# Kernel tuning notes

Hardware: AMD Instinct MI355X
Metric: run time of the kernel (lower is better)

## Reference

```python
import jax, jax.numpy as jnp
import numpy as np

C = 128  # hidden_dim


def setup_inputs() -> dict:
    key = jax.random.key(0)
    ks = jax.random.split(key, 8)
    B, H, W = 4, 64, 64
    x1 = jax.random.normal(ks[0], (B, C, H, W), dtype=jnp.float32)
    x2 = jax.random.normal(ks[1], (B, C, H, W), dtype=jnp.float32)
    # 1x1 conv == per-pixel linear over channels; store weights as [C_out, C_in]
    s = 1.0 / np.sqrt(C)
    wq = jax.random.uniform(ks[2], (C, C), jnp.float32, -s, s)
    bq = jax.random.uniform(ks[3], (C,), jnp.float32, -s, s)
    wk = jax.random.uniform(ks[4], (C, C), jnp.float32, -s, s)
    bk = jax.random.uniform(ks[5], (C,), jnp.float32, -s, s)
    wv = jax.random.uniform(ks[6], (C, C), jnp.float32, -s, s)
    bv = jax.random.uniform(ks[7], (C,), jnp.float32, -s, s)
    return {"x1": x1, "x2": x2, "wq": wq, "bq": bq, "wk": wk, "bk": bk, "wv": wv, "bv": bv}


def reference(x1, x2, wq, bq, wk, bk, wv, bv):
    B, Cc, H, W = x1.shape
    N = H * W
    # flatten spatial -> tokens: [B, N, C]
    t1 = x1.reshape(B, Cc, N).transpose(0, 2, 1)
    t2 = x2.reshape(B, Cc, N).transpose(0, 2, 1)
    # 1x1 conv projections (per-token linear)
    q = jnp.einsum('bnc,oc->bno', t1, wq) + bq
    k = jnp.einsum('bnc,oc->bno', t2, wk) + bk
    v = jnp.einsum('bnc,oc->bno', t2, wv) + bv
    scale = 1.0 / jnp.sqrt(jnp.asarray(Cc, x1.dtype))
    attn = jax.nn.softmax(jnp.einsum('bqc,bkc->bqk', q, k) * scale, axis=-1)
    out = jnp.einsum('bqk,bkc->bqc', attn, v)  # [B, N, C]
    out = out.transpose(0, 2, 1).reshape(B, Cc, H, W)
    return out + x1
```

## Files before the change

### kernel.cpp

```cpp
#include <hip/hip_runtime.h>
#include <hip/hip_bf16.h>

typedef float  f32x4  __attribute__((ext_vector_type(4)));
typedef float  f32x16 __attribute__((ext_vector_type(16)));
typedef short  s16x8  __attribute__((ext_vector_type(8)));
typedef int    i32x8  __attribute__((ext_vector_type(8)));
typedef unsigned int   u32x2 __attribute__((ext_vector_type(2)));
typedef unsigned int   u32x4 __attribute__((ext_vector_type(4)));

#define B_ 4
#define C_ 128
#define N_ 4096
#define NST 16
#define QSCALE 0.12751744f

__device__ __forceinline__ unsigned int pkbf(float lo, float hi) {
    union { float f; unsigned int u; } a, b; a.f = lo; b.f = hi;
    return __builtin_amdgcn_perm(b.u + 0x8000u, a.u + 0x8000u, 0x07060302u);
}
__device__ __forceinline__ unsigned int pk_fp8x4(float a, float b, float c, float d) {
    int v = __builtin_amdgcn_cvt_pk_fp8_f32(a, b, 0, false);
    v = __builtin_amdgcn_cvt_pk_fp8_f32(c, d, v, true);
    return (unsigned int)v;
}
__device__ __forceinline__ s16x8 mk_frag(unsigned int a, unsigned int b,
                                         unsigned int c, unsigned int d) {
    union { u32x4 u; s16x8 v; } t; t.u = (u32x4){a, b, c, d}; return t.v;
}
__device__ __forceinline__ f32x16 z16() {
    f32x16 v;
    #pragma unroll
    for (int r = 0; r < 16; r++) v[r] = 0.f;
    return v;
}
__device__ __forceinline__ i32x8 ld32g(const unsigned char* p) {
    union { u32x4 q[2]; i32x8 v; } t;
    t.q[0] = *(const u32x4*)p;
    t.q[1] = *(const u32x4*)(p + 1024);
    return t.v;
}
__device__ __forceinline__ f32x16 mfs(i32x8 a, i32x8 b, f32x16 c) {
    return __builtin_amdgcn_mfma_scale_f32_32x32x64_f8f6f4(
        a, b, c, 0, 0, 0, 0x7F7F7F7Fu, 0, 0x7F7F7F7Fu);
}

__global__ __launch_bounds__(256) void wcvt_kernel(
    const float* __restrict__ wq, const float* __restrict__ wk,
    const float* __restrict__ wv, unsigned short* __restrict__ Wf)
{
    const int gid = blockIdx.x * 256 + threadIdx.x;
    const int l = gid & 63, fid = gid >> 6;
    const int kc = fid & 7, ot = (fid >> 3) & 3, z = fid >> 5;
    const float* w = (z == 0) ? wq : (z == 1 ? wk : wv);
    const int o  = 32 * ot + (l & 31);
    const int c0 = 16 * kc + 8 * (l >> 5);
    const float* src = &w[o * C_ + c0];
    *(u32x4*)&Wf[fid * 512 + l * 8] = (u32x4){
        pkbf(src[0], src[1]), pkbf(src[2], src[3]),
        pkbf(src[4], src[5]), pkbf(src[6], src[7])};
}

__global__ __launch_bounds__(256, 2) void proj_kernel(
    const float* __restrict__ x1, const float* __restrict__ x2,
    const float* __restrict__ bq, const float* __restrict__ bk,
    const float* __restrict__ bv,
    const unsigned short* __restrict__ Wf,
    unsigned char* __restrict__ Qf, unsigned char* __restrict__ Kf,
    unsigned char* __restrict__ Vf)
{
    __shared__ float Xs[2][C_ * 36];
    const int tid = threadIdx.x;
    const int ot  = tid >> 6;
    const int l = tid & 63, lo = l & 31, h = l >> 5;
    const int bid = blockIdx.x;
    const int b = bid & 3, tb = bid >> 2;
    const int n0 = tb * 32;

    {
        const int q = tid & 7, c0 = tid >> 3;
        #pragma unroll
        for (int cc = 0; cc < 4; cc++) {
            const int c = c0 + 32 * cc;
            const size_t gof = ((size_t)b * C_ + c) * N_ + n0 + 4 * q;
            *(f32x4*)&Xs[0][c * 36 + 4 * q] = *(const f32x4*)&x1[gof];
            *(f32x4*)&Xs[1][c * 36 + 4 * q] = *(const f32x4*)&x2[gof];
        }
    }
    __syncthreads();

    auto ldW = [&](int z, int kc) -> s16x8 {
        return *(const s16x8*)&Wf[(((z * 4 + ot) * 8) + kc) * 512 + l * 8];
    };
    auto xfrag = [&](int z, int kc) -> s16x8 {
        const float* p = &Xs[z][(16 * kc + 8 * h) * 36 + lo];
        float f[8];
        #pragma unroll
        for (int i = 0; i < 8; i++) f[i] = p[i * 36];
        return mk_frag(pkbf(f[0], f[1]), pkbf(f[2], f[3]),
                       pkbf(f[4], f[5]), pkbf(f[6], f[7]));
    };

    f32x16 aq = z16(), ak = z16(), av = z16();
    s16x8 wqA = ldW(0, 0), wkA = ldW(1, 0), wvA = ldW(2, 0);
    s16x8 wqB, wkB, wvB;
    #pragma unroll
    for (int kc = 0; kc < 8; kc++) {
        if (kc & 1) {
            if (kc < 7) { wqA = ldW(0, kc + 1); wkA = ldW(1, kc + 1); wvA = ldW(2, kc + 1); }
            s16x8 f1 = xfrag(0, kc), f2 = xfrag(1, kc);
            aq = __builtin_amdgcn_mfma_f32_32x32x16_bf16(wqB, f1, aq, 0, 0, 0);
            ak = __builtin_amdgcn_mfma_f32_32x32x16_bf16(wkB, f2, ak, 0, 0, 0);
            av = __builtin_amdgcn_mfma_f32_32x32x16_bf16(f2, wvB, av, 0, 0, 0);
        } else {
            if (kc < 7) { wqB = ldW(0, kc + 1); wkB = ldW(1, kc + 1); wvB = ldW(2, kc + 1); }
            s16x8 f1 = xfrag(0, kc), f2 = xfrag(1, kc);
            aq = __builtin_amdgcn_mfma_f32_32x32x16_bf16(wqA, f1, aq, 0, 0, 0);
            ak = __builtin_amdgcn_mfma_f32_32x32x16_bf16(wkA, f2, ak, 0, 0, 0);
            av = __builtin_amdgcn_mfma_f32_32x32x16_bf16(f2, wvA, av, 0, 0, 0);
        }
    }

    const size_t fbase = (size_t)(b * 128 + tb) * 4096;
    #pragma unroll
    for (int rq = 0; rq < 4; rq++) {
        const int o0 = 32 * ot + 8 * rq + 4 * h;
        const f32x4 b4q = *(const f32x4*)&bq[o0];
        const f32x4 b4k = *(const f32x4*)&bk[o0];
        const size_t off = fbase + (ot >> 1) * 2048 + (rq >> 1) * 1024
                         + ((ot & 1) * 32 + lo) * 16 + 8 * (rq & 1) + 4 * h;
        *(unsigned int*)&Qf[off] = pk_fp8x4(
            (aq[4*rq+0] + b4q[0]) * QSCALE, (aq[4*rq+1] + b4q[1]) * QSCALE,
            (aq[4*rq+2] + b4q[2]) * QSCALE, (aq[4*rq+3] + b4q[3]) * QSCALE);
        *(unsigned int*)&Kf[off] = pk_fp8x4(
            ak[4*rq+0] + b4k[0], ak[4*rq+1] + b4k[1],
            ak[4*rq+2] + b4k[2], ak[4*rq+3] + b4k[3]);
    }
    {
        const float bvv = bv[32 * ot + lo];
        const size_t vbase = ((size_t)(b * 64 + (tb >> 1)) * 4 + ot) * 2048;
        #pragma unroll
        for (int rq = 0; rq < 4; rq++) {
            const size_t off = vbase + (rq >> 1) * 1024
                             + ((tb & 1) * 32 + lo) * 16 + 8 * (rq & 1) + 4 * h;
            *(unsigned int*)&Vf[off] = pk_fp8x4(
                av[4*rq+0] + bvv, av[4*rq+1] + bvv,
                av[4*rq+2] + bvv, av[4*rq+3] + bvv);
        }
    }
}

__global__ __launch_bounds__(512, 2) void attn_kernel(
    const unsigned char* __restrict__ Qf,
    const unsigned char* __restrict__ Kf,
    const unsigned char* __restrict__ Vf,
    const float* __restrict__ x1,
    float* __restrict__ out)
{
    __shared__ float Ol[4 * 128 * 33];
    __shared__ float Llds[8][32];

    const int tid = threadIdx.x;
    const int w  = tid >> 6;
    const int qi = w & 1, ps = w >> 1;
    const int l = tid & 63, lo = l & 31, h = l >> 5;
    const int bid = blockIdx.x;
    const int xcd = bid & 7, slot = bid >> 3;
    const int b  = xcd >> 1;
    const int qt = ((xcd & 1) << 5) | slot;
    const int q0 = qt * 64;

    const unsigned char* Kb = Kf + (size_t)b * 524288 + 2 * ps * 4096 + l * 16;
    const unsigned char* Vb = Vf + (size_t)b * 524288 + ps * 8192 + l * 16;

    i32x8 qb0, qb1;
    {
        const unsigned char* qp = Qf + (size_t)(b * 128 + qt * 2 + qi) * 4096 + l * 16;
        qb0 = ld32g(qp);
        qb1 = ld32g(qp + 2048);
    }

    f32x16 oacc[4];
    #pragma unroll
    for (int ct = 0; ct < 4; ct++) oacc[ct] = z16();
    float La = 0.f, Lb2 = 0.f;

    i32x8 k0, k1, k2, k3;
    {
        const unsigned char* Kg = Kb + (size_t)(slot & 15) * 32768;
        k0 = ld32g(Kg);        k1 = ld32g(Kg + 2048);
        k2 = ld32g(Kg + 4096); k3 = ld32g(Kg + 6144);
    }

    #pragma unroll
    for (int t = 0; t < NST; t++) {
        const int tp = (t + slot) & 15;
        const unsigned char* Vg = Vb + (size_t)tp * 32768;
        i32x8 v0 = ld32g(Vg);        i32x8 v1 = ld32g(Vg + 2048);
        i32x8 v2 = ld32g(Vg + 4096); i32x8 v3 = ld32g(Vg + 6144);
        i32x8 n0, n1, n2, n3;
        if (t + 1 < NST) {
            const unsigned char* Kg = Kb + (size_t)((t + 1 + slot) & 15) * 32768;
            n0 = ld32g(Kg);        n1 = ld32g(Kg + 2048);
            n2 = ld32g(Kg + 4096); n3 = ld32g(Kg + 6144);
        }
        f32x16 s0 = z16(), s1 = z16();
        s0 = mfs(k0, qb0, s0);
        s0 = mfs(k1, qb1, s0);
        s1 = mfs(k2, qb0, s1);
        s1 = mfs(k3, qb1, s1);
        float e0[16], e1[16];
        #pragma unroll
        for (int r = 0; r < 16; r++) {
            e0[r] = __builtin_amdgcn_exp2f(s0[r]);
            e1[r] = __builtin_amdgcn_exp2f(s1[r]);
        }
        #pragma unroll
        for (int r = 0; r < 8; r++) { La += e0[r] + e1[r]; Lb2 += e0[r+8] + e1[r+8]; }
        union { unsigned int u[8]; i32x8 v; } pb;
        #pragma unroll
        for (int j = 0; j < 4; j++) {
            const unsigned int w0 = pk_fp8x4(e0[4*j], e0[4*j+1], e0[4*j+2], e0[4*j+3]);
            const unsigned int w1 = pk_fp8x4(e1[4*j], e1[4*j+1], e1[4*j+2], e1[4*j+3]);
            u32x2 sw = __builtin_amdgcn_permlane32_swap(w0, w1, false, false);
            pb.u[2*j]   = sw[0];
            pb.u[2*j+1] = sw[1];
        }
        const i32x8 pB = pb.v;
        oacc[0] = mfs(v0, pB, oacc[0]);
        oacc[1] = mfs(v1, pB, oacc[1]);
        oacc[2] = mfs(v2, pB, oacc[2]);
        oacc[3] = mfs(v3, pB, oacc[3]);
        k0 = n0; k1 = n1; k2 = n2; k3 = n3;
    }

    const float Lh = La + Lb2;
    const float Lsum = Lh + __shfl_xor(Lh, 32, 64);
    if (l < 32) Llds[w][lo] = Lsum;
    __syncthreads();

    for (int g = 0; g < 2; g++) {
        if (qi == g) {
            #pragma unroll
            for (int ct = 0; ct < 4; ct++)
                #pragma unroll
                for (int r = 0; r < 16; r++) {
                    const int c = 32 * ct + (r & 3) + 8 * (r >> 2) + 4 * h;
                    Ol[ps * 4224 + c * 33 + lo] = oacc[ct][r];
                }
        }
        __syncthreads();
        {
            const int c = tid >> 2, qq = tid & 3;
            const size_t gbase = ((size_t)b * C_ + c) * N_ + q0 + g * 32 + qq * 8;
            float v[8];
            #pragma unroll
            for (int j = 0; j < 8; j++) {
                const int q = qq * 8 + j;
                const float ssum = Ol[c * 33 + q]        + Ol[4224  + c * 33 + q]
                                 + Ol[8448 + c * 33 + q] + Ol[12672 + c * 33 + q];
                const float Lq = Llds[g][q] + Llds[2 + g][q]
                               + Llds[4 + g][q] + Llds[6 + g][q];
                v[j] = ssum * __builtin_amdgcn_rcpf(Lq);
            }
            const f32x4 xlo = *(const f32x4*)&x1[gbase];
            const f32x4 xhi = *(const f32x4*)&x1[gbase + 4];
            *(f32x4*)&out[gbase]     = (f32x4){v[0]+xlo[0], v[1]+xlo[1], v[2]+xlo[2], v[3]+xlo[3]};
            *(f32x4*)&out[gbase + 4] = (f32x4){v[4]+xhi[0], v[5]+xhi[1], v[6]+xhi[2], v[7]+xhi[3]};
        }
        __syncthreads();
    }
}

extern "C" void kernel_launch(void* const* d_in, const int* in_sizes, int n_in,
                              void* d_out, int out_size, void* d_ws, size_t ws_size,
                              hipStream_t stream)
{
    const float* x1 = (const float*)d_in[0];
    const float* x2 = (const float*)d_in[1];
    const float* wq = (const float*)d_in[2];
    const float* bq = (const float*)d_in[3];
    const float* wk = (const float*)d_in[4];
    const float* bk = (const float*)d_in[5];
    const float* wv = (const float*)d_in[6];
    const float* bv = (const float*)d_in[7];
    float* out = (float*)d_out;

    unsigned short* Wf = (unsigned short*)d_ws;
    unsigned char* Qf = (unsigned char*)d_ws + 98304;
    unsigned char* Kf = Qf + (size_t)B_ * 128 * 4096;
    unsigned char* Vf = Kf + (size_t)B_ * 128 * 4096;

    wcvt_kernel<<<24, 256, 0, stream>>>(wq, wk, wv, Wf);
    proj_kernel<<<512, 256, 0, stream>>>(x1, x2, bq, bk, bv, Wf, Qf, Kf, Vf);
    attn_kernel<<<256, 512, 0, stream>>>(Qf, Kf, Vf, x1, out);
}
```

Before: 42.52 us.

## Have each wave process both query subtiles over its own key slice to reuse K/V

Each wave now holds both 32-query subtiles of the block and iterates over an exclusive eighth of the keys, instead of one query subtile over a quarter of the keys. Each loaded K and V fragment therefore feeds two sets of MFMAs, roughly halving global K/V traffic per block. The main loop is also set to no unroll, with loads interleaved between the two softmax stages. In exchange the wave carries twice the accumulators, which raises register pressure, and the epilogue needs an extra LDS accumulation pass plus a barrier to combine eight partial sums.

Result: slower. 121.9 us (+186.7%).

```diff
diff --git a/kernel.cpp b/kernel.cpp
--- a/kernel.cpp
+++ b/kernel.cpp
@@ -11,7 +11,6 @@
 #define B_ 4
 #define C_ 128
 #define N_ 4096
-#define NST 16
 #define QSCALE 0.12751744f
 
 __device__ __forceinline__ unsigned int pkbf(float lo, float hi) {
@@ -157,11 +156,10 @@
     float* __restrict__ out)
 {
     __shared__ float Ol[4 * 128 * 33];
-    __shared__ float Llds[8][32];
+    __shared__ float Llds[8][2][32];
 
     const int tid = threadIdx.x;
     const int w  = tid >> 6;
-    const int qi = w & 1, ps = w >> 1;
     const int l = tid & 63, lo = l & 31, h = l >> 5;
     const int bid = blockIdx.x;
     const int xcd = bid & 7, slot = bid >> 3;
@@ -169,45 +167,23 @@
     const int qt = ((xcd & 1) << 5) | slot;
     const int q0 = qt * 64;
 
-    const unsigned char* Kb = Kf + (size_t)b * 524288 + 2 * ps * 4096 + l * 16;
-    const unsigned char* Vb = Vf + (size_t)b * 524288 + ps * 8192 + l * 16;
-
-    i32x8 qb0, qb1;
-    {
-        const unsigned char* qp = Qf + (size_t)(b * 128 + qt * 2 + qi) * 4096 + l * 16;
-        qb0 = ld32g(qp);
-        qb1 = ld32g(qp + 2048);
-    }
-
-    f32x16 oacc[4];
+    const unsigned char* Kb = Kf + (size_t)b * 524288 + (size_t)w * 65536 + l * 16;
+    const unsigned char* Vb = Vf + (size_t)b * 524288 + (size_t)w * 65536 + l * 16;
+
+    i32x8 qA0, qA1, qB0, qB1;
+    {
+        const unsigned char* qp = Qf + (size_t)(b * 128 + qt * 2) * 4096 + l * 16;
+        qA0 = ld32g(qp);        qA1 = ld32g(qp + 2048);
+        qB0 = ld32g(qp + 4096); qB1 = ld32g(qp + 6144);
+    }
+
+    f32x16 oA[4], oB[4];
     #pragma unroll
-    for (int ct = 0; ct < 4; ct++) oacc[ct] = z16();
-    float La = 0.f, Lb2 = 0.f;
-
-    i32x8 k0, k1, k2, k3;
-    {
-        const unsigned char* Kg = Kb + (size_t)(slot & 15) * 32768;
-        k0 = ld32g(Kg);        k1 = ld32g(Kg + 2048);
-        k2 = ld32g(Kg + 4096); k3 = ld32g(Kg + 6144);
-    }
-
-    #pragma unroll
-    for (int t = 0; t < NST; t++) {
-        const int tp = (t + slot) & 15;
-        const unsigned char* Vg = Vb + (size_t)tp * 32768;
-        i32x8 v0 = ld32g(Vg);        i32x8 v1 = ld32g(Vg + 2048);
-        i32x8 v2 = ld32g(Vg + 4096); i32x8 v3 = ld32g(Vg + 6144);
-        i32x8 n0, n1, n2, n3;
-        if (t + 1 < NST) {
-            const unsigned char* Kg = Kb + (size_t)((t + 1 + slot) & 15) * 32768;
-            n0 = ld32g(Kg);        n1 = ld32g(Kg + 2048);
-            n2 = ld32g(Kg + 4096); n3 = ld32g(Kg + 6144);
-        }
-        f32x16 s0 = z16(), s1 = z16();
-        s0 = mfs(k0, qb0, s0);
-        s0 = mfs(k1, qb1, s0);
-        s1 = mfs(k2, qb0, s1);
-        s1 = mfs(k3, qb1, s1);
+    for (int ct = 0; ct < 4; ct++) { oA[ct] = z16(); oB[ct] = z16(); }
+    float LaA = 0.f, LbA = 0.f, LaB = 0.f, LbB = 0.f;
+
+    auto softmax_pack = [&](const f32x16& s0, const f32x16& s1,
+                            float& La, float& Lb) -> i32x8 {
         float e0[16], e1[16];
         #pragma unroll
         for (int r = 0; r < 16; r++) {
@@ -215,7 +191,7 @@
             e1[r] = __builtin_amdgcn_exp2f(s1[r]);
         }
         #pragma unroll
-        for (int r = 0; r < 8; r++) { La += e0[r] + e1[r]; Lb2 += e0[r+8] + e1[r+8]; }
+        for (int r = 0; r < 8; r++) { La += e0[r] + e1[r]; Lb += e0[r+8] + e1[r+8]; }
         union { unsigned int u[8]; i32x8 v; } pb;
         #pragma unroll
         for (int j = 0; j < 4; j++) {
@@ -225,27 +201,74 @@
             pb.u[2*j]   = sw[0];
             pb.u[2*j+1] = sw[1];
         }
-        const i32x8 pB = pb.v;
-        oacc[0] = mfs(v0, pB, oacc[0]);
-        oacc[1] = mfs(v1, pB, oacc[1]);
-        oacc[2] = mfs(v2, pB, oacc[2]);
-        oacc[3] = mfs(v3, pB, oacc[3]);
-        k0 = n0; k1 = n1; k2 = n2; k3 = n3;
-    }
-
-    const float Lh = La + Lb2;
-    const float Lsum = Lh + __shfl_xor(Lh, 32, 64);
-    if (l < 32) Llds[w][lo] = Lsum;
+        return pb.v;
+    };
+
+    i32x8 k0, k1, k2, k3;
+    {
+        const unsigned char* Kg = Kb + (size_t)(slot & 7) * 8192;
+        k0 = ld32g(Kg);        k1 = ld32g(Kg + 2048);
+        k2 = ld32g(Kg + 4096); k3 = ld32g(Kg + 6144);
+    }
+
+    #pragma unroll 1
+    for (int t = 0; t < 8; t++) {
+        const int tp = (t + slot) & 7;
+        const unsigned char* Vg = Vb + (size_t)tp * 8192;
+        f32x16 sA0 = z16(), sA1 = z16();
+        sA0 = mfs(k0, qA0, sA0);
+        sA0 = mfs(k1, qA1, sA0);
+        sA1 = mfs(k2, qA0, sA1);
+        sA1 = mfs(k3, qA1, sA1);
+        const i32x8 pA = softmax_pack(sA0, sA1, LaA, LbA);
+        i32x8 v0 = ld32g(Vg);
+        i32x8 v1 = ld32g(Vg + 2048);
+        f32x16 sB0 = z16(), sB1 = z16();
+        sB0 = mfs(k0, qB0, sB0);
+        sB0 = mfs(k1, qB1, sB0);
+        sB1 = mfs(k2, qB0, sB1);
+        sB1 = mfs(k3, qB1, sB1);
+        i32x8 v2 = ld32g(Vg + 4096);
+        i32x8 v3 = ld32g(Vg + 6144);
+        const i32x8 pB = softmax_pack(sB0, sB1, LaB, LbB);
+        if (t + 1 < 8) {
+            const unsigned char* Kg = Kb + (size_t)((t + 1 + slot) & 7) * 8192;
+            k0 = ld32g(Kg);        k1 = ld32g(Kg + 2048);
+            k2 = ld32g(Kg + 4096); k3 = ld32g(Kg + 6144);
+        }
+        oA[0] = mfs(v0, pA, oA[0]);  oB[0] = mfs(v0, pB, oB[0]);
+        oA[1] = mfs(v1, pA, oA[1]);  oB[1] = mfs(v1, pB, oB[1]);
+        oA[2] = mfs(v2, pA, oA[2]);  oB[2] = mfs(v2, pB, oB[2]);
+        oA[3] = mfs(v3, pA, oA[3]);  oB[3] = mfs(v3, pB, oB[3]);
+    }
+
+    {
+        const float LA = LaA + LbA, LB = LaB + LbB;
+        const float LAs = LA + __shfl_xor(LA, 32, 64);
+        const float LBs = LB + __shfl_xor(LB, 32, 64);
+        if (l < 32) { Llds[w][0][lo] = LAs; Llds[w][1][lo] = LBs; }
+    }
     __syncthreads();
 
     for (int g = 0; g < 2; g++) {
-        if (qi == g) {
+        const f32x16* oc = (g == 0) ? oA : oB;
+        if (w < 4) {
             #pragma unroll
             for (int ct = 0; ct < 4; ct++)
                 #pragma unroll
                 for (int r = 0; r < 16; r++) {
                     const int c = 32 * ct + (r & 3) + 8 * (r >> 2) + 4 * h;
-                    Ol[ps * 4224 + c * 33 + lo] = oacc[ct][r];
+                    Ol[w * 4224 + c * 33 + lo] = oc[ct][r];
+                }
+        }
+        __syncthreads();
+        if (w >= 4) {
+            #pragma unroll
+            for (int ct = 0; ct < 4; ct++)
+                #pragma unroll
+                for (int r = 0; r < 16; r++) {
+                    const int c = 32 * ct + (r & 3) + 8 * (r >> 2) + 4 * h;
+                    Ol[(w - 4) * 4224 + c * 33 + lo] += oc[ct][r];
                 }
         }
         __syncthreads();
@@ -258,8 +281,9 @@
                 const int q = qq * 8 + j;
                 const float ssum = Ol[c * 33 + q]        + Ol[4224  + c * 33 + q]
                                  + Ol[8448 + c * 33 + q] + Ol[12672 + c * 33 + q];
-                const float Lq = Llds[g][q] + Llds[2 + g][q]
-                               + Llds[4 + g][q] + Llds[6 + g][q];
+                float Lq = 0.f;
+                #pragma unroll
+                for (int s8 = 0; s8 < 8; s8++) Lq += Llds[s8][g][q];
                 v[j] = ssum * __builtin_amdgcn_rcpf(Lq);
             }
             const f32x4 xlo = *(const f32x4*)&x1[gbase];
```

## Software-pipeline attention loop so PV MFMA overlaps next QK and softmax

Applied to the files above, without the earlier changes.

Restructures the attention inner loop into a prologue/steady-state/epilogue form. Each iteration now interleaves the PV MFMAs of the previous tile with the QK MFMAs of the current tile, and the exp/fp8 packing runs after them. The aim is to hide MFMA latency and the softmax dependency chain behind independent matrix work. In exchange it keeps more registers live (V, K and P at once), and the loop unroll drops from full to 2, which could affect scheduling.

Result: no change. 42.23 us (-0.7%).

```diff
diff --git a/kernel.cpp b/kernel.cpp
--- a/kernel.cpp
+++ b/kernel.cpp
@@ -184,30 +184,7 @@
     for (int ct = 0; ct < 4; ct++) oacc[ct] = z16();
     float La = 0.f, Lb2 = 0.f;
 
-    i32x8 k0, k1, k2, k3;
-    {
-        const unsigned char* Kg = Kb + (size_t)(slot & 15) * 32768;
-        k0 = ld32g(Kg);        k1 = ld32g(Kg + 2048);
-        k2 = ld32g(Kg + 4096); k3 = ld32g(Kg + 6144);
-    }
-
-    #pragma unroll
-    for (int t = 0; t < NST; t++) {
-        const int tp = (t + slot) & 15;
-        const unsigned char* Vg = Vb + (size_t)tp * 32768;
-        i32x8 v0 = ld32g(Vg);        i32x8 v1 = ld32g(Vg + 2048);
-        i32x8 v2 = ld32g(Vg + 4096); i32x8 v3 = ld32g(Vg + 6144);
-        i32x8 n0, n1, n2, n3;
-        if (t + 1 < NST) {
-            const unsigned char* Kg = Kb + (size_t)((t + 1 + slot) & 15) * 32768;
-            n0 = ld32g(Kg);        n1 = ld32g(Kg + 2048);
-            n2 = ld32g(Kg + 4096); n3 = ld32g(Kg + 6144);
-        }
-        f32x16 s0 = z16(), s1 = z16();
-        s0 = mfs(k0, qb0, s0);
-        s0 = mfs(k1, qb1, s0);
-        s1 = mfs(k2, qb0, s1);
-        s1 = mfs(k3, qb1, s1);
+    auto softmax_pack = [&](const f32x16& s0, const f32x16& s1) -> i32x8 {
         float e0[16], e1[16];
         #pragma unroll
         for (int r = 0; r < 16; r++) {
@@ -225,13 +202,54 @@
             pb.u[2*j]   = sw[0];
             pb.u[2*j+1] = sw[1];
         }
-        const i32x8 pB = pb.v;
+        return pb.v;
+    };
+
+    i32x8 k0, k1, k2, k3, v0, v1, v2, v3, pB;
+
+    {
+        const unsigned char* Kg = Kb + (size_t)(slot & 15) * 32768;
+        k0 = ld32g(Kg);        k1 = ld32g(Kg + 2048);
+        k2 = ld32g(Kg + 4096); k3 = ld32g(Kg + 6144);
+        f32x16 s0 = z16(), s1 = z16();
+        s0 = mfs(k0, qb0, s0);
+        s0 = mfs(k1, qb1, s0);
+        s1 = mfs(k2, qb0, s1);
+        s1 = mfs(k3, qb1, s1);
+        const unsigned char* Vg = Vb + (size_t)(slot & 15) * 32768;
+        v0 = ld32g(Vg);        v1 = ld32g(Vg + 2048);
+        v2 = ld32g(Vg + 4096); v3 = ld32g(Vg + 6144);
+        const unsigned char* Kn = Kb + (size_t)((1 + slot) & 15) * 32768;
+        k0 = ld32g(Kn);        k1 = ld32g(Kn + 2048);
+        k2 = ld32g(Kn + 4096); k3 = ld32g(Kn + 6144);
+        pB = softmax_pack(s0, s1);
+    }
+
+    #pragma unroll 2
+    for (int t = 1; t < NST; t++) {
+        f32x16 s0 = z16(), s1 = z16();
         oacc[0] = mfs(v0, pB, oacc[0]);
+        s0 = mfs(k0, qb0, s0);
         oacc[1] = mfs(v1, pB, oacc[1]);
+        s0 = mfs(k1, qb1, s0);
         oacc[2] = mfs(v2, pB, oacc[2]);
+        s1 = mfs(k2, qb0, s1);
         oacc[3] = mfs(v3, pB, oacc[3]);
-        k0 = n0; k1 = n1; k2 = n2; k3 = n3;
-    }
+        s1 = mfs(k3, qb1, s1);
+        const unsigned char* Vg = Vb + (size_t)((t + slot) & 15) * 32768;
+        v0 = ld32g(Vg);        v1 = ld32g(Vg + 2048);
+        v2 = ld32g(Vg + 4096); v3 = ld32g(Vg + 6144);
+        if (t + 1 < NST) {
+            const unsigned char* Kn = Kb + (size_t)((t + 1 + slot) & 15) * 32768;
+            k0 = ld32g(Kn);        k1 = ld32g(Kn + 2048);
+            k2 = ld32g(Kn + 4096); k3 = ld32g(Kn + 6144);
+        }
+        pB = softmax_pack(s0, s1);
+    }
+    oacc[0] = mfs(v0, pB, oacc[0]);
+    oacc[1] = mfs(v1, pB, oacc[1]);
+    oacc[2] = mfs(v2, pB, oacc[2]);
+    oacc[3] = mfs(v3, pB, oacc[3]);
 
     const float Lh = La + Lb2;
     const float Lsum = Lh + __shfl_xor(Lh, 32, 64);
```

## Software-pipeline attention loop to overlap QK, softmax, and PV MFMA stages

Applied to the files above, without the earlier changes.

Restructures the per-tile inner loop into a staggered software pipeline. QK MFMAs for the next half-tile, exp/fp8 packing for the current one, and PV MFMAs for the previous one are interleaved, with K and V loads split into halves and issued just ahead of use. The goal is to hide exp and global-load latency behind matrix work instead of running each stage serially per tile. The loop is no longer fully unrolled, and the explicit prologue and epilogue scheduling is more complex and more sensitive to register pressure.

Result: no change. 42.08 us (-1.0%).

```diff
diff --git a/kernel.cpp b/kernel.cpp
--- a/kernel.cpp
+++ b/kernel.cpp
@@ -11,7 +11,6 @@
 #define B_ 4
 #define C_ 128
 #define N_ 4096
-#define NST 16
 #define QSCALE 0.12751744f
 
 __device__ __forceinline__ unsigned int pkbf(float lo, float hi) {
@@ -184,54 +183,85 @@
     for (int ct = 0; ct < 4; ct++) oacc[ct] = z16();
     float La = 0.f, Lb2 = 0.f;
 
-    i32x8 k0, k1, k2, k3;
-    {
-        const unsigned char* Kg = Kb + (size_t)(slot & 15) * 32768;
-        k0 = ld32g(Kg);        k1 = ld32g(Kg + 2048);
-        k2 = ld32g(Kg + 4096); k3 = ld32g(Kg + 6144);
-    }
-
-    #pragma unroll
-    for (int t = 0; t < NST; t++) {
-        const int tp = (t + slot) & 15;
-        const unsigned char* Vg = Vb + (size_t)tp * 32768;
-        i32x8 v0 = ld32g(Vg);        i32x8 v1 = ld32g(Vg + 2048);
-        i32x8 v2 = ld32g(Vg + 4096); i32x8 v3 = ld32g(Vg + 6144);
-        i32x8 n0, n1, n2, n3;
-        if (t + 1 < NST) {
-            const unsigned char* Kg = Kb + (size_t)((t + 1 + slot) & 15) * 32768;
-            n0 = ld32g(Kg);        n1 = ld32g(Kg + 2048);
-            n2 = ld32g(Kg + 4096); n3 = ld32g(Kg + 6144);
-        }
-        f32x16 s0 = z16(), s1 = z16();
-        s0 = mfs(k0, qb0, s0);
-        s0 = mfs(k1, qb1, s0);
-        s1 = mfs(k2, qb0, s1);
-        s1 = mfs(k3, qb1, s1);
-        float e0[16], e1[16];
-        #pragma unroll
-        for (int r = 0; r < 16; r++) {
-            e0[r] = __builtin_amdgcn_exp2f(s0[r]);
-            e1[r] = __builtin_amdgcn_exp2f(s1[r]);
-        }
-        #pragma unroll
-        for (int r = 0; r < 8; r++) { La += e0[r] + e1[r]; Lb2 += e0[r+8] + e1[r+8]; }
-        union { unsigned int u[8]; i32x8 v; } pb;
-        #pragma unroll
-        for (int j = 0; j < 4; j++) {
-            const unsigned int w0 = pk_fp8x4(e0[4*j], e0[4*j+1], e0[4*j+2], e0[4*j+3]);
-            const unsigned int w1 = pk_fp8x4(e1[4*j], e1[4*j+1], e1[4*j+2], e1[4*j+3]);
-            u32x2 sw = __builtin_amdgcn_permlane32_swap(w0, w1, false, false);
-            pb.u[2*j]   = sw[0];
-            pb.u[2*j+1] = sw[1];
-        }
-        const i32x8 pB = pb.v;
-        oacc[0] = mfs(v0, pB, oacc[0]);
-        oacc[1] = mfs(v1, pB, oacc[1]);
-        oacc[2] = mfs(v2, pB, oacc[2]);
-        oacc[3] = mfs(v3, pB, oacc[3]);
-        k0 = n0; k1 = n1; k2 = n2; k3 = n3;
-    }
+    i32x8 k0a, k0b, k1a, k1b;
+    i32x8 va0, va1, vb0, vb1;
+    i32x8 pb;
+    f32x16 sE, sO;
+    unsigned int w0s, w1s, w2s, w3s;
+
+    auto kaddr = [&](int j) -> const unsigned char* {
+        return Kb + (size_t)(((j >> 1) + slot) & 15) * 32768 + (size_t)(j & 1) * 4096;
+    };
+    auto vaddr = [&](int p) -> const unsigned char* {
+        return Vb + (size_t)((p + slot) & 15) * 32768;
+    };
+    auto ldK0 = [&](int j) { const unsigned char* p = kaddr(j); k0a = ld32g(p); k0b = ld32g(p + 2048); };
+    auto ldK1 = [&](int j) { const unsigned char* p = kaddr(j); k1a = ld32g(p); k1b = ld32g(p + 2048); };
+    auto ldVa = [&](int p) { const unsigned char* q = vaddr(p); va0 = ld32g(q);        va1 = ld32g(q + 2048); };
+    auto ldVb = [&](int p) { const unsigned char* q = vaddr(p); vb0 = ld32g(q + 4096); vb1 = ld32g(q + 6144); };
+
+    auto qkE = [&]() { f32x16 s = z16(); s = mfs(k0a, qb0, s); sE = mfs(k0b, qb1, s); };
+    auto qkO = [&]() { f32x16 s = z16(); s = mfs(k1a, qb0, s); sO = mfs(k1b, qb1, s); };
+
+    auto smE_ = [&]() {
+        float e[16];
+        #pragma unroll
+        for (int r = 0; r < 16; r++) e[r] = __builtin_amdgcn_exp2f(sE[r]);
+        #pragma unroll
+        for (int r = 0; r < 8; r++) { La += e[r]; Lb2 += e[r + 8]; }
+        w0s = pk_fp8x4(e[0],  e[1],  e[2],  e[3]);
+        w1s = pk_fp8x4(e[4],  e[5],  e[6],  e[7]);
+        w2s = pk_fp8x4(e[8],  e[9],  e[10], e[11]);
+        w3s = pk_fp8x4(e[12], e[13], e[14], e[15]);
+    };
+    auto smO_ = [&]() {
+        float e[16];
+        #pragma unroll
+        for (int r = 0; r < 16; r++) e[r] = __builtin_amdgcn_exp2f(sO[r]);
+        #pragma unroll
+        for (int r = 0; r < 8; r++) { La += e[r]; Lb2 += e[r + 8]; }
+        const unsigned int x0 = pk_fp8x4(e[0],  e[1],  e[2],  e[3]);
+        const unsigned int x1v = pk_fp8x4(e[4],  e[5],  e[6],  e[7]);
+        const unsigned int x2 = pk_fp8x4(e[8],  e[9],  e[10], e[11]);
+        const unsigned int x3 = pk_fp8x4(e[12], e[13], e[14], e[15]);
+        u32x2 s0w = __builtin_amdgcn_permlane32_swap(w0s, x0,  false, false);
+        u32x2 s1w = __builtin_amdgcn_permlane32_swap(w1s, x1v, false, false);
+        u32x2 s2w = __builtin_amdgcn_permlane32_swap(w2s, x2,  false, false);
+        u32x2 s3w = __builtin_amdgcn_permlane32_swap(w3s, x3,  false, false);
+        union { unsigned int u[8]; i32x8 v; } t;
+        t.u[0] = s0w[0]; t.u[1] = s0w[1]; t.u[2] = s1w[0]; t.u[3] = s1w[1];
+        t.u[4] = s2w[0]; t.u[5] = s2w[1]; t.u[6] = s3w[0]; t.u[7] = s3w[1];
+        pb = t.v;
+    };
+
+    auto pv01 = [&]() { oacc[0] = mfs(va0, pb, oacc[0]); oacc[1] = mfs(va1, pb, oacc[1]); };
+    auto pv23 = [&]() { oacc[2] = mfs(vb0, pb, oacc[2]); oacc[3] = mfs(vb1, pb, oacc[3]); };
+
+    ldK0(0); ldK1(1);
+    qkE();
+    qkO(); ldK0(2); smE_();
+    qkE(); ldVa(0); ldK1(3); smO_();
+    pv01(); qkO(); ldVb(0); ldK0(4); smE_();
+
+    for (int m = 2; m <= 15; m++) {
+        pv23();
+        qkE();
+        ldVa(m - 1);
+        ldK1(2 * m + 1);
+        smO_();
+        pv01();
+        qkO();
+        ldVb(m - 1);
+        if (m < 15) ldK0(2 * m + 2);
+        smE_();
+    }
+
+    pv23();
+    ldVa(15);
+    smO_();
+    pv01();
+    ldVb(15);
+    pv23();
 
     const float Lh = La + Lb2;
     const float Lsum = Lh + __shfl_xor(Lh, 32, 64);
```
